# Optimization experiments

Measured on AMD Instinct MI355X. Metric: run time of the kernel, lower is better.

Reference implementation:

```python
import jax, jax.numpy as jnp
import numpy as np

N_NODES = 50000
N_EDGES = 800000
N_GRAPHS = 64
C = 32          # hidden channels per irrep
L = 3           # message-passing layers
NB = 10         # radial basis size
MAX_RADIUS = 2.5
DEG_NORM = 4.0  # sqrt(num_neighbors=16)
EPS = 1e-8


def radial_basis(d):
    # soft one-hot Gaussian basis over [0, MAX_RADIUS], shape [E, NB]
    x = jnp.clip(d / MAX_RADIUS, 0.0, 1.0)
    centers = jnp.linspace(0.0, 1.0, NB)
    return jnp.exp(-((x[:, None] - centers[None, :]) * NB) ** 2)


def setup_inputs() -> dict:
    key = jax.random.key(0)
    ks = jax.random.split(key, 16)
    pos = jax.random.normal(ks[0], (N_NODES, 3), dtype=jnp.float32)
    node_feats = jax.random.normal(ks[1], (N_NODES, 4), dtype=jnp.float32)
    edge_src = jax.random.randint(ks[2], (N_EDGES,), 0, N_NODES)
    edge_dst = jax.random.randint(ks[3], (N_EDGES,), 0, N_NODES)
    batch = jnp.sort(jax.random.randint(ks[4], (N_NODES,), 0, N_GRAPHS))
    W_emb = jax.random.normal(ks[5], (4, C), dtype=jnp.float32) / np.sqrt(4.0)
    Wr1 = jax.random.normal(ks[6], (L, NB, 64), dtype=jnp.float32) / np.sqrt(NB)
    Wr2 = jax.random.normal(ks[7], (L, 64, 5 * C), dtype=jnp.float32) / np.sqrt(64.0)
    W1 = jax.random.normal(ks[8], (L, C, C), dtype=jnp.float32) / np.sqrt(C)
    W2 = jax.random.normal(ks[9], (L, C, C), dtype=jnp.float32) / np.sqrt(C)
    U1 = jax.random.normal(ks[10], (L, C, C), dtype=jnp.float32) / np.sqrt(C)
    U2 = jax.random.normal(ks[11], (L, C, C), dtype=jnp.float32) / np.sqrt(C)
    w_out = jax.random.normal(ks[12], (C,), dtype=jnp.float32) / np.sqrt(C)
    return {"pos": pos, "node_feats": node_feats, "edge_src": edge_src,
            "edge_dst": edge_dst, "batch": batch, "W_emb": W_emb,
            "Wr1": Wr1, "Wr2": Wr2, "W1": W1, "W2": W2,
            "U1": U1, "U2": U2, "w_out": w_out}


def _forward(pos, node_feats, W_emb, Wr1, Wr2, W1, W2, U1, U2, w_out,
             edge_src, edge_dst, batch):
    # initial embedding: scalar (0e) channels; vector (1o) channels start at 0
    s = node_feats @ W_emb                      # [N, C]
    v = jnp.zeros((s.shape[0], C, 3), s.dtype)  # [N, C, 3]

    r = pos[edge_dst] - pos[edge_src]           # [E, 3] relative positions
    d = jnp.sqrt(jnp.sum(r * r, axis=-1) + EPS)
    u = r / d[:, None]                          # unit vectors ~ l=1 SH
    rb = radial_basis(d)                        # [E, NB]

    for l in range(L):
        # radial MLP -> per-edge, per-path, per-channel tensor-product weights
        h = jax.nn.silu(rb @ Wr1[l]) @ Wr2[l]   # [E, 5*C]
        h = h.reshape(-1, 5, C)
        s_j = s[edge_src]                       # [E, C] gather
        v_j = v[edge_src]                       # [E, C, 3] gather
        # equivariant TP paths: 0e x Y0 -> 0e ; 0e x Y1 -> 1o ;
        # 1o x Y0 -> 1o ; 1o . Y1 -> 0e ; 1o x Y1 -> 1o (cross)
        m_s = h[:, 0] * s_j + h[:, 3] * jnp.einsum('ecd,ed->ec', v_j, u)
        m_v = (h[:, 1][..., None] * s_j[..., None] * u[:, None, :]
               + h[:, 2][..., None] * v_j
               + h[:, 4][..., None] * jnp.cross(v_j, u[:, None, :]))
        agg_s = jax.ops.segment_sum(m_s, edge_dst, num_segments=s.shape[0]) / DEG_NORM
        agg_v = jax.ops.segment_sum(m_v, edge_dst, num_segments=s.shape[0]) / DEG_NORM
        # self-interaction (channel mixing) + gated nonlinearity
        s_upd = s @ W1[l] + agg_s @ W2[l]
        v_upd = jnp.einsum('ncd,cf->nfd', v, U1[l]) + jnp.einsum('ncd,cf->nfd', agg_v, U2[l])
        s = jax.nn.silu(s_upd)
        v = v_upd * jax.nn.sigmoid(s_upd)[..., None]

    # average pooling per graph
    counts = jax.ops.segment_sum(jnp.ones_like(s[:, 0]), batch, num_segments=N_GRAPHS)
    counts = jnp.maximum(counts, 1.0)
    v_pool = jax.ops.segment_sum(v, batch, num_segments=N_GRAPHS) / counts[:, None, None]
    u3 = jnp.einsum('gcd,c->gd', v_pool, w_out)  # 1x1o output [G, 3]
    return u3[:, :2]                             # wrapper slice u_3D[..., :2]


def reference(pos, node_feats, edge_src, edge_dst, batch, W_emb,
              Wr1, Wr2, W1, W2, U1, U2, w_out):
    return _forward(pos, node_feats, W_emb, Wr1, Wr2, W1, W2, U1, U2, w_out,
                    edge_src, edge_dst, batch)
```

## Files before the change

kernel.cpp:

```cpp
#include <hip/hip_runtime.h>
#include <math.h>

#define NN 50000
#define NE 800000
#define NG 64
#define NC 32
#define NL 3
#define NBASIS 10
#define LUT_M 4096
#define LUT_ROWS (LUT_M + 1)
#define CAP 52
#define JT 16
#define JBLK ((LUT_ROWS + JT - 1) / JT)
#define LUT_BLOCKS (NL * JBLK)
#define EMB_BLOCKS ((NN*NC + 255)/256)
#define GEO_BLOCKS ((NE + 255)/256)

__device__ inline unsigned short f2b(float f) {
    unsigned int x = __float_as_uint(f);
    return (unsigned short)((x + 0x7FFFu + ((x >> 16) & 1u)) >> 16);
}
__device__ inline float lo16(unsigned int w) { return __uint_as_float(w << 16); }
__device__ inline float hi16(unsigned int w) { return __uint_as_float(w & 0xFFFF0000u); }

#define ST0_OFF   0u
#define ST1_OFF   12800000u
#define GEOR_OFF  25600000u
#define LUT0_OFF  67200000u
#define LUTC_OFF  67724416u
#define CUR_OFF   71919744u
#define WS_NEED   72119744u

__global__ void prologue_kernel(const float* __restrict__ Wr1, const float* __restrict__ Wr2,
                                unsigned int* __restrict__ lut0, uint4* __restrict__ lutc,
                                const float* __restrict__ nf, const float* __restrict__ Wemb,
                                uint2* __restrict__ st,
                                const float* __restrict__ pos, const int* __restrict__ esrc,
                                const int* __restrict__ edst, int* __restrict__ cursor,
                                float4* __restrict__ geoR)
{
    int bid = blockIdx.x;
    int t = threadIdx.x;
    if (bid < LUT_BLOCKS) {
        __shared__ float w2s[64*160];
        __shared__ float w1s[NBASIS*64];
        __shared__ float hid[JT][64];
        int l  = bid / JBLK;
        int jb = (bid % JBLK) * JT;
        for (int i = t; i < 64*160; i += 256)    w2s[i] = Wr2[l*64*160 + i];
        for (int i = t; i < NBASIS*64; i += 256) w1s[i] = Wr1[l*NBASIS*64 + i];
        __syncthreads();
        for (int task = t; task < JT*64; task += 256) {
            int jl = task >> 6, k = task & 63;
            int j = jb + jl;
            if (j <= LUT_M) {
                float x = (float)j * (1.0f / (float)LUT_M);
                float acc = 0.0f;
                #pragma unroll
                for (int b = 0; b < NBASIS; b++) {
                    float z = (x - (float)b * (1.0f/9.0f)) * 10.0f;
                    acc += expf(-z*z) * w1s[b*64 + k];
                }
                hid[jl][k] = acc / (1.0f + expf(-acc));
            }
        }
        __syncthreads();
        for (int task = t; task < JT*32; task += 256) {
            int jl = task >> 5, c = task & 31;
            int j = jb + jl;
            if (j > LUT_M) continue;
            float a0=0.f, a1=0.f, a2=0.f, a3=0.f, a4=0.f;
            #pragma unroll 8
            for (int k = 0; k < 64; k++) {
                float h = hid[jl][k];
                const float* wr = w2s + k*160 + c;
                a0 += h*wr[0];  a1 += h*wr[32]; a2 += h*wr[64];
                a3 += h*wr[96]; a4 += h*wr[128];
            }
            a0 *= 0.25f; a1 *= 0.25f; a2 *= 0.25f; a3 *= 0.25f; a4 *= 0.25f;
            unsigned int h01 = (unsigned int)f2b(a0) | ((unsigned int)f2b(a1) << 16);
            if (l == 0) {
                lut0[(size_t)j*32 + c] = h01;
            } else {
                lutc[((size_t)(l-1)*LUT_ROWS + j)*32 + c] = make_uint4(
                    h01,
                    (unsigned int)f2b(a2) | ((unsigned int)f2b(a3) << 16),
                    (unsigned int)f2b(a4), 0u);
            }
        }
    } else if (bid < LUT_BLOCKS + EMB_BLOCKS) {
        int i = (bid - LUT_BLOCKS) * 256 + t;
        if (i < NN*NC) {
            int n = i >> 5, f = i & 31;
            float4 x = ((const float4*)nf)[n];
            float s = x.x*Wemb[f] + x.y*Wemb[NC+f] + x.z*Wemb[2*NC+f] + x.w*Wemb[3*NC+f];
            st[i] = make_uint2((unsigned int)f2b(s), 0u);
        }
    } else {
        int e = (bid - LUT_BLOCKS - EMB_BLOCKS) * 256 + t;
        if (e < NE) {
            int s = esrc[e], d = edst[e];
            float rx = pos[3*d+0] - pos[3*s+0];
            float ry = pos[3*d+1] - pos[3*s+1];
            float rz = pos[3*d+2] - pos[3*s+2];
            float dd = sqrtf(rx*rx + ry*ry + rz*rz + 1e-8f);
            float inv = 1.0f / dd;
            float tt = fminf(dd * (1.0f/2.5f), 1.0f) * (float)LUT_M;
            int j = min((int)(tt + 0.5f), LUT_M);
            unsigned int rec = (unsigned int)j | ((unsigned int)s << 14);
            int p = atomicAdd(&cursor[d], 1);
            if (p < CAP)
                geoR[(size_t)d*CAP + p] = make_float4(__uint_as_float(rec), rx*inv, ry*inv, rz*inv);
        }
    }
}

template<bool FIRST>
__global__ void fused_kernel(const uint2* __restrict__ stIn,
                             uint2* __restrict__ stOut,
                             const float4* __restrict__ geoR,
                             const int* __restrict__ cursor,
                             const unsigned int* __restrict__ lut0,
                             const uint4* __restrict__ lutc,
                             const float* __restrict__ W1, const float* __restrict__ W2,
                             const float* __restrict__ U1, const float* __restrict__ U2)
{
    __shared__ uint2 wp[NC][NC];
    __shared__ float4 mbA[8][NC];
    __shared__ float4 mbB[8][NC];
    for (int i = threadIdx.x; i < NC*NC; i += 256) {
        wp[i >> 5][i & 31] = make_uint2(
            (unsigned int)f2b(W1[i]) | ((unsigned int)f2b(W2[i]) << 16),
            (unsigned int)f2b(U1[i]) | ((unsigned int)f2b(U2[i]) << 16));
    }
    __syncthreads();

    int lane = threadIdx.x & 31;
    int sub  = threadIdx.x >> 5;
    int n = blockIdx.x * 8 + sub;

    uint2 stn = stIn[(size_t)n*NC + lane];

    int k0 = n * CAP;
    int k1 = k0 + min(cursor[n], CAP);
    float as = 0.f, a0 = 0.f, a1 = 0.f, a2 = 0.f;

    auto body = [&](const float4& g, uint2 st, uint4 H) {
        float u0 = g.y, u1 = g.z, u2 = g.w;
        float sj = lo16(st.x);
        float h0 = lo16(H.x), h1 = hi16(H.x);
        float hs = h1 * sj;
        if (FIRST) {
            as += h0*sj;
            a0 += hs*u0; a1 += hs*u1; a2 += hs*u2;
        } else {
            float h2 = lo16(H.y), h3 = hi16(H.y), h4 = lo16(H.z);
            float v0 = hi16(st.x), v1 = lo16(st.y), v2 = hi16(st.y);
            float dot = v0*u0 + v1*u1 + v2*u2;
            float c0 = v1*u2 - v2*u1;
            float c1 = v2*u0 - v0*u2;
            float c2 = v0*u1 - v1*u0;
            as += h0*sj + h3*dot;
            a0 += hs*u0 + h2*v0 + h4*c0;
            a1 += hs*u1 + h2*v1 + h4*c1;
            a2 += hs*u2 + h2*v2 + h4*c2;
        }
    };

    const uint4 zero4 = make_uint4(0u,0u,0u,0u);
    int k = k0;
    for (; k + 4 <= k1; k += 4) {
        float4 g0 = geoR[k], g1 = geoR[k+1], g2 = geoR[k+2], g3 = geoR[k+3];
        unsigned int r0 = __float_as_uint(g0.x), r1 = __float_as_uint(g1.x);
        unsigned int r2 = __float_as_uint(g2.x), r3 = __float_as_uint(g3.x);
        int j0 = r0 & 16383, s0 = r0 >> 14;
        int j1 = r1 & 16383, s1 = r1 >> 14;
        int j2 = r2 & 16383, s2 = r2 >> 14;
        int j3 = r3 & 16383, s3 = r3 >> 14;
        uint4 H0, H1, H2, H3;
        if (FIRST) {
            H0 = zero4; H1 = zero4; H2 = zero4; H3 = zero4;
            H0.x = lut0[(size_t)j0*32 + lane];
            H1.x = lut0[(size_t)j1*32 + lane];
            H2.x = lut0[(size_t)j2*32 + lane];
            H3.x = lut0[(size_t)j3*32 + lane];
        } else {
            H0 = lutc[(size_t)j0*32 + lane];
            H1 = lutc[(size_t)j1*32 + lane];
            H2 = lutc[(size_t)j2*32 + lane];
            H3 = lutc[(size_t)j3*32 + lane];
        }
        uint2 t0 = stIn[(size_t)s0*NC + lane];
        uint2 t1 = stIn[(size_t)s1*NC + lane];
        uint2 t2 = stIn[(size_t)s2*NC + lane];
        uint2 t3 = stIn[(size_t)s3*NC + lane];
        body(g0, t0, H0);
        body(g1, t1, H1);
        body(g2, t2, H2);
        body(g3, t3, H3);
    }
    for (; k < k1; k++) {
        float4 g = geoR[k];
        unsigned int r = __float_as_uint(g.x);
        int j = r & 16383, s = r >> 14;
        uint4 H;
        if (FIRST) { H = zero4; H.x = lut0[(size_t)j*32 + lane]; }
        else       { H = lutc[(size_t)j*32 + lane]; }
        uint2 st = stIn[(size_t)s*NC + lane];
        body(g, st, H);
    }

    float sv = lo16(stn.x);
    float vv0 = hi16(stn.x), vv1 = lo16(stn.y), vv2 = hi16(stn.y);
    mbA[sub][lane] = make_float4(sv, as, vv0, a0);
    mbB[sub][lane] = make_float4(vv1, a1, vv2, a2);

    float s_ = 0.f, b0 = 0.f, b1 = 0.f, b2v = 0.f;
    #pragma unroll
    for (int c = 0; c < NC; c++) {
        float4 A = mbA[sub][c];
        float4 B = mbB[sub][c];
        uint2 W = wp[c][lane];
        float w1 = lo16(W.x), w2 = hi16(W.x);
        float q1 = lo16(W.y), q2 = hi16(W.y);
        s_  += A.x*w1 + A.y*w2;
        b0  += A.z*q1 + A.w*q2;
        b1  += B.x*q1 + B.y*q2;
        b2v += B.z*q1 + B.w*q2;
    }
    float sg = 1.0f / (1.0f + expf(-s_));
    uint2 outp;
    outp.x = (unsigned int)f2b(s_ * sg) | ((unsigned int)f2b(b0*sg) << 16);
    outp.y = (unsigned int)f2b(b1*sg)   | ((unsigned int)f2b(b2v*sg) << 16);
    stOut[(size_t)n*NC + lane] = outp;
}

__global__ void pool_kernel(const uint2* __restrict__ st, const int* __restrict__ batch,
                            const float* __restrict__ wout, float* __restrict__ out)
{
    int g = blockIdx.x;
    int lane = threadIdx.x & 31;
    int sub  = threadIdx.x >> 5;
    int lo = 0, hi = NN;
    while (lo < hi) { int m = (lo + hi) >> 1; if (batch[m] < g) lo = m + 1; else hi = m; }
    int start = lo;
    hi = NN;
    while (lo < hi) { int m = (lo + hi) >> 1; if (batch[m] < g + 1) lo = m + 1; else hi = m; }
    int end = lo;

    float wv = wout[lane];
    float p0 = 0.f, p1 = 0.f;
    for (int n = start + sub; n < end; n += 8) {
        uint2 r = st[(size_t)n*NC + lane];
        p0 += hi16(r.x) * wv;
        p1 += lo16(r.y) * wv;
    }
    #pragma unroll
    for (int off = 16; off > 0; off >>= 1) {
        p0 += __shfl_xor(p0, off, 32);
        p1 += __shfl_xor(p1, off, 32);
    }
    __shared__ float red[16];
    if (lane == 0) { red[sub] = p0; red[8 + sub] = p1; }
    __syncthreads();
    if (threadIdx.x == 0) {
        float t0 = 0.f, t1 = 0.f;
        for (int i = 0; i < 8; i++) { t0 += red[i]; t1 += red[8 + i]; }
        float inv = 1.0f / fmaxf((float)(end - start), 1.0f);
        out[g*2 + 0] = t0 * inv;
        out[g*2 + 1] = t1 * inv;
    }
}

extern "C" void kernel_launch(void* const* d_in, const int* in_sizes, int n_in,
                              void* d_out, int out_size, void* d_ws, size_t ws_size,
                              hipStream_t stream)
{
    const float* pos   = (const float*)d_in[0];
    const float* nf    = (const float*)d_in[1];
    const int*   esrc  = (const int*)d_in[2];
    const int*   edst  = (const int*)d_in[3];
    const int*   batch = (const int*)d_in[4];
    const float* Wemb  = (const float*)d_in[5];
    const float* Wr1   = (const float*)d_in[6];
    const float* Wr2   = (const float*)d_in[7];
    const float* W1    = (const float*)d_in[8];
    const float* W2    = (const float*)d_in[9];
    const float* U1    = (const float*)d_in[10];
    const float* U2    = (const float*)d_in[11];
    const float* wout  = (const float*)d_in[12];

    char* ws = (char*)d_ws;
    uint2* stbuf[2] = { (uint2*)(ws + ST0_OFF), (uint2*)(ws + ST1_OFF) };
    float4* geoR = (float4*)(ws + GEOR_OFF);
    unsigned int* lut0 = (unsigned int*)(ws + LUT0_OFF);
    uint4* lutc = (uint4*)(ws + LUTC_OFF);
    int* cursor = (int*)(ws + CUR_OFF);

    hipMemsetAsync(cursor, 0, 200000u, stream);

    prologue_kernel<<<LUT_BLOCKS + EMB_BLOCKS + GEO_BLOCKS, 256, 0, stream>>>(
        Wr1, Wr2, lut0, lutc, nf, Wemb, stbuf[0], pos, esrc, edst, cursor, geoR);

    fused_kernel<true><<<NN/8, 256, 0, stream>>>(stbuf[0], stbuf[1], geoR, cursor,
                                                 lut0, lutc,
                                                 W1, W2, U1, U2);
    for (int l = 1; l < NL; l++) {
        int in = l & 1, outb = 1 - in;
        fused_kernel<false><<<NN/8, 256, 0, stream>>>(stbuf[in], stbuf[outb], geoR, cursor,
                                                      lut0,
                                                      lutc + (size_t)(l-1)*LUT_ROWS*32,
                                                      W1 + l*NC*NC, W2 + l*NC*NC,
                                                      U1 + l*NC*NC, U2 + l*NC*NC);
    }

    pool_kernel<<<NG, 256, 0, stream>>>(stbuf[NL & 1], batch, wout, (float*)d_out);
}
```

Baseline: 334.5 us.

## Sort nodes by in-degree so fused kernel blocks get balanced work

```diff
diff --git a/kernel.cpp b/kernel.cpp
--- a/kernel.cpp
+++ b/kernel.cpp
@@ -10,11 +10,13 @@
 #define LUT_M 4096
 #define LUT_ROWS (LUT_M + 1)
 #define CAP 52
+#define NBINS 53
 #define JT 16
 #define JBLK ((LUT_ROWS + JT - 1) / JT)
 #define LUT_BLOCKS (NL * JBLK)
 #define EMB_BLOCKS ((NN*NC + 255)/256)
 #define GEO_BLOCKS ((NE + 255)/256)
+#define SORT_BLOCKS ((NN + 255)/256)
 
 __device__ inline unsigned short f2b(float f) {
     unsigned int x = __float_as_uint(f);
@@ -29,7 +31,11 @@
 #define LUT0_OFF  67200000u
 #define LUTC_OFF  67724416u
 #define CUR_OFF   71919744u
-#define WS_NEED   72119744u
+#define ORD_OFF   72119744u
+#define BIN_OFF   72319744u
+#define BOF_OFF   72320000u
+#define BCU_OFF   72320256u
+#define WS_NEED   72320512u
 
 __global__ void prologue_kernel(const float* __restrict__ Wr1, const float* __restrict__ Wr2,
                                 unsigned int* __restrict__ lut0, uint4* __restrict__ lutc,
@@ -115,11 +121,53 @@
     }
 }
 
+__global__ void bin_hist_kernel(const int* __restrict__ cursor, int* __restrict__ bins)
+{
+    __shared__ int h[NBINS];
+    int t = threadIdx.x;
+    if (t < NBINS) h[t] = 0;
+    __syncthreads();
+    int n = blockIdx.x * 256 + t;
+    if (n < NN) atomicAdd(&h[min(cursor[n], CAP)], 1);
+    __syncthreads();
+    if (t < NBINS && h[t]) atomicAdd(&bins[t], h[t]);
+}
+
+__global__ void bin_scan_kernel(const int* __restrict__ bins, int* __restrict__ binoff)
+{
+    if (threadIdx.x == 0) {
+        int run = 0;
+        for (int d = NBINS - 1; d >= 0; d--) { binoff[d] = run; run += bins[d]; }
+    }
+}
+
+__global__ void order_scatter_kernel(const int* __restrict__ cursor, const int* __restrict__ binoff,
+                                     int* __restrict__ bincur, int* __restrict__ order)
+{
+    __shared__ int h[NBINS];
+    __shared__ int base[NBINS];
+    __shared__ int lcur[NBINS];
+    int t = threadIdx.x;
+    if (t < NBINS) { h[t] = 0; lcur[t] = 0; }
+    __syncthreads();
+    int n = blockIdx.x * 256 + t;
+    int d = -1;
+    if (n < NN) { d = min(cursor[n], CAP); atomicAdd(&h[d], 1); }
+    __syncthreads();
+    if (t < NBINS && h[t]) base[t] = atomicAdd(&bincur[t], h[t]);
+    __syncthreads();
+    if (n < NN) {
+        int r = atomicAdd(&lcur[d], 1);
+        order[binoff[d] + base[d] + r] = n;
+    }
+}
+
 template<bool FIRST>
 __global__ void fused_kernel(const uint2* __restrict__ stIn,
                              uint2* __restrict__ stOut,
                              const float4* __restrict__ geoR,
                              const int* __restrict__ cursor,
+                             const int* __restrict__ order,
                              const unsigned int* __restrict__ lut0,
                              const uint4* __restrict__ lutc,
                              const float* __restrict__ W1, const float* __restrict__ W2,
@@ -137,7 +185,7 @@
 
     int lane = threadIdx.x & 31;
     int sub  = threadIdx.x >> 5;
-    int n = blockIdx.x * 8 + sub;
+    int n = order[blockIdx.x * 8 + sub];
 
     uint2 stn = stIn[(size_t)n*NC + lane];
 
@@ -296,18 +344,27 @@
     unsigned int* lut0 = (unsigned int*)(ws + LUT0_OFF);
     uint4* lutc = (uint4*)(ws + LUTC_OFF);
     int* cursor = (int*)(ws + CUR_OFF);
+    int* order  = (int*)(ws + ORD_OFF);
+    int* bins   = (int*)(ws + BIN_OFF);
+    int* binoff = (int*)(ws + BOF_OFF);
+    int* bincur = (int*)(ws + BCU_OFF);
 
     hipMemsetAsync(cursor, 0, 200000u, stream);
+    hipMemsetAsync(bins, 0, 768u, stream);
 
     prologue_kernel<<<LUT_BLOCKS + EMB_BLOCKS + GEO_BLOCKS, 256, 0, stream>>>(
         Wr1, Wr2, lut0, lutc, nf, Wemb, stbuf[0], pos, esrc, edst, cursor, geoR);
 
-    fused_kernel<true><<<NN/8, 256, 0, stream>>>(stbuf[0], stbuf[1], geoR, cursor,
+    bin_hist_kernel<<<SORT_BLOCKS, 256, 0, stream>>>(cursor, bins);
+    bin_scan_kernel<<<1, 64, 0, stream>>>(bins, binoff);
+    order_scatter_kernel<<<SORT_BLOCKS, 256, 0, stream>>>(cursor, binoff, bincur, order);
+
+    fused_kernel<true><<<NN/8, 256, 0, stream>>>(stbuf[0], stbuf[1], geoR, cursor, order,
                                                  lut0, lutc,
                                                  W1, W2, U1, U2);
     for (int l = 1; l < NL; l++) {
         int in = l & 1, outb = 1 - in;
-        fused_kernel<false><<<NN/8, 256, 0, stream>>>(stbuf[in], stbuf[outb], geoR, cursor,
+        fused_kernel<false><<<NN/8, 256, 0, stream>>>(stbuf[in], stbuf[outb], geoR, cursor, order,
                                                       lut0,
                                                       lutc + (size_t)(l-1)*LUT_ROWS*32,
                                                       W1 + l*NC*NC, W2 + l*NC*NC,
```

Result: faster. 313.7 us, median of 2 (-6.2%).
